# Performance work log

Hardware: AMD Instinct MI355X
Metric: run time of the kernel (lower is better)

The kernel has to match this reference:

```python
import jax, jax.numpy as jnp
import numpy as np

N_HEADS = 4
D_HEAD = 16
SCALE = D_HEAD ** 0.5  # NOTE: original multiplies by sqrt(d_head), faithful


def _mha(x, Wq, bq, Wk, bk, Wv, bv, Wo, bo):
    # x: (..., N, D) with D = N_HEADS * D_HEAD
    q = jnp.einsum('...nd,od->...no', x, Wq) + bq
    k = jnp.einsum('...nd,od->...no', x, Wk) + bk
    v = jnp.einsum('...nd,od->...no', x, Wv) + bv
    lead = x.shape[:-2]
    n = x.shape[-2]
    q = q.reshape(*lead, n, N_HEADS, D_HEAD)
    k = k.reshape(*lead, n, N_HEADS, D_HEAD)
    v = v.reshape(*lead, n, N_HEADS, D_HEAD)
    scores = jnp.einsum('...nhd,...mhd->...hnm', q, k) * SCALE
    attn = jax.nn.softmax(scores, axis=-1)
    o = jnp.einsum('...hnm,...mhd->...nhd', attn, v).reshape(*lead, n, N_HEADS * D_HEAD)
    return jnp.einsum('...nd,od->...no', o, Wo) + bo


def setup_inputs() -> dict:
    key = jax.random.key(0)
    ks = jax.random.split(key, 20)
    b, n, d, dhf, G, C = 16, 16384, 64, 64, 256, 64
    s = 0.05
    inp = {
        'x': jax.random.normal(ks[0], (b, n, d), dtype=jnp.float32),
        'partitions': jax.random.permutation(ks[1], n).reshape(G, C).astype(jnp.int64),
    }
    names = ['q_intra', 'k_intra', 'v_intra', 'o_intra',
             'q_inter', 'k_inter', 'v_inter', 'o_inter']
    for i, nm in enumerate(names):
        d_in = d if nm.endswith('intra') and nm[0] != 'o' else dhf
        inp['W' + nm] = jax.random.normal(ks[2 + 2 * i], (dhf, d_in), dtype=jnp.float32) * s
        inp['b' + nm] = jax.random.normal(ks[3 + 2 * i], (dhf,), dtype=jnp.float32) * s
    return inp


def reference(x, partitions,
              Wq_intra, bq_intra, Wk_intra, bk_intra, Wv_intra, bv_intra, Wo_intra, bo_intra,
              Wq_inter, bq_inter, Wk_inter, bk_inter, Wv_inter, bv_inter, Wo_inter, bo_inter):
    b = x.shape[0]
    G, C = partitions.shape
    dhf = Wq_intra.shape[0]
    # gather nodes into groups: (b, G, C, d)
    xg = x[:, partitions, :]
    # intra-group attention, vectorized over (b, G)
    intra = _mha(xg, Wq_intra, bq_intra, Wk_intra, bk_intra,
                 Wv_intra, bv_intra, Wo_intra, bo_intra)  # (b, G, C, dhf)
    # MaxPool1d(kernel=dhf) over token axis with C == dhf -> max over tokens
    pooled = jnp.max(intra, axis=2)  # (b, G, dhf)
    inter = _mha(pooled, Wq_inter, bq_inter, Wk_inter, bk_inter,
                 Wv_inter, bv_inter, Wo_inter, bo_inter)  # (b, G, dhf)
    # broadcast-add inter-group features to every token in the group
    out = intra + inter[:, :, None, :]  # (b, G, C, dhf)
    flat = out.reshape(b, G * C, dhf)
    inv = jnp.argsort(partitions.reshape(-1))  # restore original node order
    return flat[:, inv, :]
```

## Files before the change

### kernel.cpp

```cpp
#include <hip/hip_runtime.h>
#include <hip/hip_bf16.h>

#define NTOK 16384
#define NG   256
#define NB   16

typedef float  f32x4   __attribute__((ext_vector_type(4)));
typedef short  short8v __attribute__((ext_vector_type(8)));
typedef short  short4v __attribute__((ext_vector_type(4)));

#define MFMA_BF16(a, b, c) __builtin_amdgcn_mfma_f32_16x16x32_bf16((a), (b), (c), 0, 0, 0)

#define QSCALE 5.770780163555856f

__device__ __forceinline__ short f2bf(float f) {
    union { float f; unsigned u; } x; x.f = f;
    unsigned r = (x.u + 0x7FFF + ((x.u >> 16) & 1)) >> 16;
    return (short)r;
}
__device__ __forceinline__ short bft(float f) {
    union { float f; unsigned u; } x; x.f = f;
    return (short)(x.u >> 16);
}
__device__ __forceinline__ float bf2f(short s) {
    union { float f; unsigned u; } x;
    x.u = ((unsigned)(unsigned short)s) << 16;
    return x.f;
}

__global__ void k_setup(const int* __restrict__ raw, int* __restrict__ part,
                        const float* __restrict__ Wq, const float* __restrict__ Wk,
                        const float* __restrict__ Wv, const float* __restrict__ Wo,
                        const float* __restrict__ Wqe, const float* __restrict__ Wke,
                        const float* __restrict__ Wve, const float* __restrict__ Woe,
                        short8v* __restrict__ wf)
{
    const int gid = blockIdx.x * 256 + threadIdx.x;
    if (gid < 16384) {
        const bool is64 = (raw[1] == 0 && raw[3] == 0 && raw[5] == 0);
        part[gid] = is64 ? raw[2 * gid] : raw[gid];
        return;
    }
    const int p = gid - 16384;
    if (p >= 5632) return;
    if (p < 3584) {
        const int v    = p >> 9;
        const int rem  = p & 511;
        const int tau  = rem >> 6;
        const int lane = rem & 63;
        const int jt = tau >> 1, kt = tau & 1;
        const int o  = jt * 16 + (lane & 15);
        const int d0 = kt * 32 + (lane >> 4) * 8;
        const float* W = (v < 2) ? Wq : (v < 4) ? Wk : (v < 6) ? Wv : Wo;
        const bool lo = (v & 1) && (v < 6);
        short8v r8;
#pragma unroll
        for (int i = 0; i < 8; ++i) {
            const float f = W[o * 64 + d0 + i];
            const short hh = f2bf(f);
            r8[i] = lo ? f2bf(f - bf2f(hh)) : hh;
        }
        wf[p] = r8;
    } else {
        const int g2   = p - 3584;
        const int v    = g2 >> 9;
        const int rem  = g2 & 511;
        const int tau  = rem >> 6;
        const int lane = rem & 63;
        const int jt = tau >> 1, kt = tau & 1;
        const int o  = jt * 16 + (lane & 15);
        const int d0 = kt * 32 + (lane >> 4) * 8;
        const float* W = (v == 0) ? Wqe : (v == 1) ? Wke : (v == 2) ? Wve : Woe;
        short8v r8;
#pragma unroll
        for (int i = 0; i < 8; ++i) r8[i] = f2bf(W[o * 64 + d0 + i]);
        wf[p] = r8;
    }
}

__global__ __launch_bounds__(256, 4) void k_intra(
    const float* __restrict__ x, const int* __restrict__ part,
    const short8v* __restrict__ wf,
    const float* __restrict__ bq, const float* __restrict__ bk,
    const float* __restrict__ bv, const float* __restrict__ bo,
    float* __restrict__ out, float* __restrict__ pooled)
{
    __shared__ __align__(16) short S[20480];

    short* const xh = S;
    short* const kk = S + 4096;
    short* const ql = S + 8192;
    short* const qh = S + 12288;
    short* const vT = S + 16384;

    const int t  = threadIdx.x;
    const int g  = blockIdx.x;
    const int bb = blockIdx.y;
    const int l  = t & 63;
    const int w  = t >> 6;
    const int quad = l >> 4;
    const int col  = l & 15;

    for (int j = t; j < 512; j += 256) {
        const int row = j >> 3, c8 = j & 7;
        const int tok = part[g * 64 + row];
        const float* px = x + ((size_t)bb * NTOK + tok) * 64 + c8 * 8;
        const float4 f0 = ((const float4*)px)[0];
        const float4 f1 = ((const float4*)px)[1];
        const float v[8] = {f0.x, f0.y, f0.z, f0.w, f1.x, f1.y, f1.z, f1.w};
        short8v h8;
#pragma unroll
        for (int i = 0; i < 8; ++i) h8[i] = f2bf(v[i]);
        *(short8v*)&xh[row * 64 + ((c8 ^ (row & 7)) << 3)] = h8;
    }
    __syncthreads();

    {
        const float bqv = bq[w * 16 + col];
        const float bkv = bk[w * 16 + col];
        const float bvv = bv[w * 16 + col];
        short8v bqh[2], bql2[2], bkh[2], bkl[2], bvh[2], bvl[2];
#pragma unroll
        for (int kt = 0; kt < 2; ++kt) {
            const int tau = w * 2 + kt;
            bqh[kt]  = wf[(0 * 8 + tau) * 64 + l];
            bql2[kt] = wf[(1 * 8 + tau) * 64 + l];
            bkh[kt]  = wf[(2 * 8 + tau) * 64 + l];
            bkl[kt]  = wf[(3 * 8 + tau) * 64 + l];
            bvh[kt]  = wf[(4 * 8 + tau) * 64 + l];
            bvl[kt]  = wf[(5 * 8 + tau) * 64 + l];
        }
        for (int mt = 0; mt < 4; ++mt) {
            short8v axh[2];
#pragma unroll
            for (int kt = 0; kt < 2; ++kt) {
                const int row = mt * 16 + col;
                axh[kt] = *(const short8v*)&xh[row * 64 + (((kt * 4 + quad) ^ (row & 7)) << 3)];
            }
            f32x4 aq = {0.f, 0.f, 0.f, 0.f};
            f32x4 ak = {0.f, 0.f, 0.f, 0.f};
            f32x4 av = {0.f, 0.f, 0.f, 0.f};
#pragma unroll
            for (int kt = 0; kt < 2; ++kt) {
                aq = MFMA_BF16(axh[kt], bqh[kt],  aq);
                aq = MFMA_BF16(axh[kt], bql2[kt], aq);
                ak = MFMA_BF16(axh[kt], bkh[kt],  ak);
                ak = MFMA_BF16(axh[kt], bkl[kt],  ak);
                av = MFMA_BF16(axh[kt], bvh[kt],  av);
                av = MFMA_BF16(axh[kt], bvl[kt],  av);
            }
#pragma unroll
            for (int r = 0; r < 4; ++r) {
                const int m = mt * 16 + quad * 4 + r;
                const int pos = m * 64 + (((w * 2 + (col >> 3)) ^ (m & 7)) << 3) + (col & 7);
                const float q4 = (aq[r] + bqv) * QSCALE;
                const short hq = bft(q4);
                qh[pos] = hq;
                ql[pos] = bft(q4 - bf2f(hq));
                kk[pos] = f2bf(ak[r] + bkv);
            }
            {
                const int d = w * 16 + col;
                short4v v4;
#pragma unroll
                for (int r = 0; r < 4; ++r) v4[r] = f2bf(av[r] + bvv);
                const int cm = mt * 2 + (quad >> 1);
                const int idx = d * 64 + ((cm ^ (d & 7)) << 3) + ((quad & 1) * 4);
                *(short4v*)&vT[idx] = v4;
            }
        }
    }

    const int h = w, hc = h * 16;
    f32x4 s[4][4];
    {
        short8v bk4[4];
#pragma unroll
        for (int jt = 0; jt < 4; ++jt) {
            const int row = jt * 16 + col;
            bk4[jt] = *(const short8v*)&kk[row * 64 + (((h * 2 + (quad & 1)) ^ (row & 7)) << 3)];
        }
        const short8v z8 = {0, 0, 0, 0, 0, 0, 0, 0};
        for (int it = 0; it < 4; ++it) {
            const int row = it * 16 + col;
            const int idx = row * 64 + (((h * 2 + (quad & 1)) ^ (row & 7)) << 3);
            short8v aqh = *(const short8v*)&qh[idx];
            short8v aql = *(const short8v*)&ql[idx];
            if (quad >= 2) { aqh = z8; aql = z8; }
#pragma unroll
            for (int jt = 0; jt < 4; ++jt) {
                f32x4 acc = {0.f, 0.f, 0.f, 0.f};
                acc = MFMA_BF16(aqh, bk4[jt], acc);
                acc = MFMA_BF16(aql, bk4[jt], acc);
                s[it][jt] = acc;
            }
        }
    }
    float rden[4][4];
    for (int it = 0; it < 4; ++it) {
#pragma unroll
        for (int r = 0; r < 4; ++r) {
            float mx = fmaxf(fmaxf(s[it][0][r], s[it][1][r]),
                             fmaxf(s[it][2][r], s[it][3][r]));
            mx = fmaxf(mx, __shfl_xor(mx, 1));
            mx = fmaxf(mx, __shfl_xor(mx, 2));
            mx = fmaxf(mx, __shfl_xor(mx, 4));
            mx = fmaxf(mx, __shfl_xor(mx, 8));
            float ds = 0.f;
#pragma unroll
            for (int jt = 0; jt < 4; ++jt) {
                const float e = exp2f(s[it][jt][r] - mx);
                s[it][jt][r] = e;
                ds += e;
            }
            ds += __shfl_xor(ds, 1);
            ds += __shfl_xor(ds, 2);
            ds += __shfl_xor(ds, 4);
            ds += __shfl_xor(ds, 8);
            rden[it][r] = 1.0f / ds;
        }
    }
    __syncthreads();

    f32x4 oa[4];
#pragma unroll
    for (int it = 0; it < 4; ++it) oa[it] = (f32x4){0.f, 0.f, 0.f, 0.f};
    short* const Pw = S + w * 2560;
    for (int kt = 0; kt < 2; ++kt) {
        for (int it = 0; it < 4; ++it)
#pragma unroll
            for (int jl = 0; jl < 2; ++jl) {
                const int jt = kt * 2 + jl;
#pragma unroll
                for (int r = 0; r < 4; ++r)
                    Pw[(it * 16 + quad * 4 + r) * 40 + jl * 16 + col] = bft(s[it][jt][r]);
            }
        const int dv = hc + col;
        const int cmv = kt * 4 + quad;
        const short8v bv8 = *(const short8v*)&vT[dv * 64 + ((cmv ^ (dv & 7)) << 3)];
        for (int it = 0; it < 4; ++it) {
            const short8v ap = *(const short8v*)&Pw[(it * 16 + col) * 40 + quad * 8];
            oa[it] = MFMA_BF16(ap, bv8, oa[it]);
        }
    }
    for (int it = 0; it < 4; ++it)
#pragma unroll
        for (int r = 0; r < 4; ++r) {
            const int row = it * 16 + quad * 4 + r;
            const int pos = row * 64 + (((h * 2 + (col >> 3)) ^ (row & 7)) << 3) + (col & 7);
            qh[pos] = f2bf(oa[it][r] * rden[it][r]);
        }
    __syncthreads();

    {
        const float bov = bo[w * 16 + col];
        short8v bo8[2];
        bo8[0] = wf[(6 * 8 + w * 2 + 0) * 64 + l];
        bo8[1] = wf[(6 * 8 + w * 2 + 1) * 64 + l];
        float pm = -1e30f;
        for (int mt = 0; mt < 4; ++mt) {
            f32x4 acc = {0.f, 0.f, 0.f, 0.f};
#pragma unroll
            for (int kt = 0; kt < 2; ++kt) {
                const int row = mt * 16 + col;
                const short8v ao = *(const short8v*)&qh[row * 64 + (((kt * 4 + quad) ^ (row & 7)) << 3)];
                acc = MFMA_BF16(ao, bo8[kt], acc);
            }
#pragma unroll
            for (int r = 0; r < 4; ++r) {
                const float vo = acc[r] + bov;
                pm = fmaxf(pm, vo);
                const int tok = part[g * 64 + mt * 16 + quad * 4 + r];
                out[((size_t)bb * NTOK + tok) * 64 + w * 16 + col] = vo;
            }
        }
        pm = fmaxf(pm, __shfl_xor(pm, 16));
        pm = fmaxf(pm, __shfl_xor(pm, 32));
        if (l < 16)
            pooled[((size_t)bb * NG + g) * 64 + w * 16 + col] = pm;
    }
}

__global__ __launch_bounds__(256) void k_inter_qkv(
    const float* __restrict__ pooled, const short8v* __restrict__ wf,
    const float* __restrict__ bq, const float* __restrict__ bk,
    const float* __restrict__ bv,
    short* __restrict__ qws, short* __restrict__ kws, short* __restrict__ vTws)
{
    __shared__ __align__(16) short xs[4096];
    __shared__ __align__(16) short qs[64 * 72];
    __shared__ __align__(16) short ks2[64 * 72];
    const int t = threadIdx.x;
    const int chunk = blockIdx.x, bb = blockIdx.y;
    const int l = t & 63, w = t >> 6;
    const int quad = l >> 4, col = l & 15;

    for (int j = t; j < 512; j += 256) {
        const int row = j >> 3, c8 = j & 7;
        const float* px = pooled + ((size_t)bb * NG + chunk * 64 + row) * 64 + c8 * 8;
        const float4 f0 = ((const float4*)px)[0];
        const float4 f1 = ((const float4*)px)[1];
        const float v[8] = {f0.x, f0.y, f0.z, f0.w, f1.x, f1.y, f1.z, f1.w};
        short8v h8;
#pragma unroll
        for (int i = 0; i < 8; ++i) h8[i] = f2bf(v[i]);
        *(short8v*)&xs[row * 64 + ((c8 ^ (row & 7)) << 3)] = h8;
    }
    __syncthreads();

    const int WFI = 3584;
    short8v bqf[2], bkf[2], bvf[2];
#pragma unroll
    for (int kt = 0; kt < 2; ++kt) {
        bqf[kt] = wf[WFI + (0 * 8 + w * 2 + kt) * 64 + l];
        bkf[kt] = wf[WFI + (1 * 8 + w * 2 + kt) * 64 + l];
        bvf[kt] = wf[WFI + (2 * 8 + w * 2 + kt) * 64 + l];
    }
    const float bqv = bq[w * 16 + col];
    const float bkv = bk[w * 16 + col];
    const float bvv = bv[w * 16 + col];
    for (int mt = 0; mt < 4; ++mt) {
        short8v ax[2];
#pragma unroll
        for (int kt = 0; kt < 2; ++kt) {
            const int row = mt * 16 + col;
            ax[kt] = *(const short8v*)&xs[row * 64 + (((kt * 4 + quad) ^ (row & 7)) << 3)];
        }
        f32x4 aq = {0.f, 0.f, 0.f, 0.f};
        f32x4 ak = {0.f, 0.f, 0.f, 0.f};
        f32x4 av = {0.f, 0.f, 0.f, 0.f};
#pragma unroll
        for (int kt = 0; kt < 2; ++kt) {
            aq = MFMA_BF16(ax[kt], bqf[kt], aq);
            ak = MFMA_BF16(ax[kt], bkf[kt], ak);
            av = MFMA_BF16(ax[kt], bvf[kt], av);
        }
        short4v v4;
#pragma unroll
        for (int r = 0; r < 4; ++r) {
            const int m = mt * 16 + quad * 4 + r;
            qs[m * 72 + w * 16 + col]  = f2bf((aq[r] + bqv) * QSCALE);
            ks2[m * 72 + w * 16 + col] = f2bf(ak[r] + bkv);
            v4[r] = f2bf(av[r] + bvv);
        }
        *(short4v*)&vTws[((size_t)bb * 64 + w * 16 + col) * 256 + chunk * 64 + mt * 16 + quad * 4] = v4;
    }
    __syncthreads();
    for (int j = t; j < 512; j += 256) {
        const int row = j >> 3, c8 = j & 7;
        *(short8v*)&qws[((size_t)bb * NG + chunk * 64 + row) * 64 + c8 * 8] =
            *(const short8v*)&qs[row * 72 + c8 * 8];
        *(short8v*)&kws[((size_t)bb * NG + chunk * 64 + row) * 64 + c8 * 8] =
            *(const short8v*)&ks2[row * 72 + c8 * 8];
    }
}

__global__ __launch_bounds__(256) void k_inter_attn2(
    const short* __restrict__ qws, const short* __restrict__ kws,
    const short* __restrict__ vTws, const short8v* __restrict__ wf,
    const float* __restrict__ bo, float* __restrict__ inter)
{
    __shared__ __align__(16) short Pw_all[4 * 16 * 40];
    __shared__ __align__(16) short os[16 * 72];
    const int t = threadIdx.x;
    const int qt = blockIdx.x, bb = blockIdx.y;
    const int l = t & 63, w = t >> 6;
    const int quad = l >> 4, col = l & 15;
    const int hc = w * 16;
    const int r0 = qt * 16;

    const short8v z8 = {0, 0, 0, 0, 0, 0, 0, 0};
    short8v bk[16];
#pragma unroll
    for (int jt = 0; jt < 16; ++jt)
        bk[jt] = (quad < 2)
            ? *(const short8v*)&kws[((size_t)bb * NG + jt * 16 + col) * 64 + hc + quad * 8]
            : z8;
    short8v aq = (quad < 2)
        ? *(const short8v*)&qws[((size_t)bb * NG + r0 + col) * 64 + hc + quad * 8]
        : z8;

    f32x4 s[16];
#pragma unroll
    for (int jt = 0; jt < 16; ++jt) {
        f32x4 acc = {0.f, 0.f, 0.f, 0.f};
        s[jt] = MFMA_BF16(aq, bk[jt], acc);
    }

    float rden[4];
#pragma unroll
    for (int r = 0; r < 4; ++r) {
        float mx = -1e30f;
#pragma unroll
        for (int jt = 0; jt < 16; ++jt) mx = fmaxf(mx, s[jt][r]);
        mx = fmaxf(mx, __shfl_xor(mx, 1));
        mx = fmaxf(mx, __shfl_xor(mx, 2));
        mx = fmaxf(mx, __shfl_xor(mx, 4));
        mx = fmaxf(mx, __shfl_xor(mx, 8));
        float ds = 0.f;
#pragma unroll
        for (int jt = 0; jt < 16; ++jt) {
            const float e = exp2f(s[jt][r] - mx);
            s[jt][r] = e;
            ds += e;
        }
        ds += __shfl_xor(ds, 1);
        ds += __shfl_xor(ds, 2);
        ds += __shfl_xor(ds, 4);
        ds += __shfl_xor(ds, 8);
        rden[r] = 1.0f / ds;
    }

    short* const Pw = Pw_all + w * 16 * 40;
    f32x4 oa = {0.f, 0.f, 0.f, 0.f};
    for (int c = 0; c < 8; ++c) {
#pragma unroll
        for (int jl = 0; jl < 2; ++jl) {
            const int jt = c * 2 + jl;
#pragma unroll
            for (int r = 0; r < 4; ++r)
                Pw[(quad * 4 + r) * 40 + jl * 16 + col] = bft(s[jt][r]);
        }
        const short8v bv8 = *(const short8v*)&vTws[((size_t)bb * 64 + hc + col) * 256 + c * 32 + quad * 8];
        const short8v ap = *(const short8v*)&Pw[col * 40 + quad * 8];
        oa = MFMA_BF16(ap, bv8, oa);
    }
#pragma unroll
    for (int r = 0; r < 4; ++r)
        os[(quad * 4 + r) * 72 + hc + col] = f2bf(oa[r] * rden[r]);
    __syncthreads();

    short8v bof[2];
    bof[0] = wf[3584 + (3 * 8 + w * 2 + 0) * 64 + l];
    bof[1] = wf[3584 + (3 * 8 + w * 2 + 1) * 64 + l];
    const float bov = bo[w * 16 + col];
    {
        f32x4 acc = {0.f, 0.f, 0.f, 0.f};
#pragma unroll
        for (int kt = 0; kt < 2; ++kt) {
            const short8v ao = *(const short8v*)&os[col * 72 + kt * 32 + quad * 8];
            acc = MFMA_BF16(ao, bof[kt], acc);
        }
#pragma unroll
        for (int r = 0; r < 4; ++r)
            inter[((size_t)bb * NG + r0 + quad * 4 + r) * 64 + w * 16 + col] = acc[r] + bov;
    }
}

__global__ __launch_bounds__(256) void k_scatter_add(
    const float* __restrict__ inter, const int* __restrict__ part,
    float* __restrict__ out)
{
    __shared__ float iv[64];
    __shared__ int   pidx[64];
    const int t  = threadIdx.x;
    const int g  = blockIdx.x;
    const int bb = blockIdx.y;
    if (t < 64) {
        iv[t]   = inter[((size_t)bb * NG + g) * 64 + t];
        pidx[t] = part[g * 64 + t];
    }
    __syncthreads();
    const int oo   = t & 63;
    const int cseg = t >> 6;
    const float add = iv[oo];
    for (int ci = 0; ci < 16; ++ci) {
        const int c = cseg * 16 + ci;
        float* p = out + ((size_t)bb * NTOK + pidx[c]) * 64 + oo;
        *p += add;
    }
}

extern "C" void kernel_launch(void* const* d_in, const int* in_sizes, int n_in,
                              void* d_out, int out_size, void* d_ws, size_t ws_size,
                              hipStream_t stream)
{
    const float* x    = (const float*)d_in[0];
    const int*   praw = (const int*)d_in[1];
    const float* Wq_a = (const float*)d_in[2];
    const float* bq_a = (const float*)d_in[3];
    const float* Wk_a = (const float*)d_in[4];
    const float* bk_a = (const float*)d_in[5];
    const float* Wv_a = (const float*)d_in[6];
    const float* bv_a = (const float*)d_in[7];
    const float* Wo_a = (const float*)d_in[8];
    const float* bo_a = (const float*)d_in[9];
    const float* Wq_e = (const float*)d_in[10];
    const float* bq_e = (const float*)d_in[11];
    const float* Wk_e = (const float*)d_in[12];
    const float* bk_e = (const float*)d_in[13];
    const float* Wv_e = (const float*)d_in[14];
    const float* bv_e = (const float*)d_in[15];
    const float* Wo_e = (const float*)d_in[16];
    const float* bo_e = (const float*)d_in[17];

    char* ws = (char*)d_ws;
    int*     part   = (int*)ws;
    float*   pooled = (float*)(ws + (1u << 16));
    float*   inter  = (float*)(ws + (1u << 16) + (1u << 20));
    short8v* wf     = (short8v*)(ws + (1u << 16) + 2 * (1u << 20));
    char*    base2  = ws + (1u << 16) + 2 * (1u << 20) + 98304;
    short*   qws    = (short*)base2;
    short*   kws    = (short*)(base2 + (1u << 19));
    short*   vTws   = (short*)(base2 + 2 * (1u << 19));

    float* out = (float*)d_out;

    k_setup<<<dim3(86), dim3(256), 0, stream>>>(praw, part, Wq_a, Wk_a, Wv_a, Wo_a,
                                                Wq_e, Wk_e, Wv_e, Wo_e, wf);
    k_intra<<<dim3(NG, NB), dim3(256), 0, stream>>>(
        x, part, wf, bq_a, bk_a, bv_a, bo_a, out, pooled);
    k_inter_qkv<<<dim3(4, NB), dim3(256), 0, stream>>>(
        pooled, wf, bq_e, bk_e, bv_e, qws, kws, vTws);
    k_inter_attn2<<<dim3(16, NB), dim3(256), 0, stream>>>(
        qws, kws, vTws, wf, bo_e, inter);
    k_scatter_add<<<dim3(NG, NB), dim3(256), 0, stream>>>(inter, part, out);
}
```

Before: 223.6 us.

## Stage intra output as grouped bf16 and scatter once in final kernel

When the workspace is large enough, the intra kernel writes its output contiguously per group as bf16 into a staging buffer instead of scattering fp32 to out. A new final kernel reads that buffer, adds the inter-group features, and writes out once in scattered order. The old path read back and rewrote out, so this cuts intermediate traffic. The bf16 rounding of intra adds precision loss. fp32 to bf16 packing now uses a perm-based paired RNE conversion.

```diff
diff --git a/kernel.cpp b/kernel.cpp
--- a/kernel.cpp
+++ b/kernel.cpp
@@ -26,6 +26,12 @@
     union { float f; unsigned u; } x;
     x.u = ((unsigned)(unsigned short)s) << 16;
     return x.f;
+}
+__device__ __forceinline__ unsigned pk_rne(float a, float b) {
+    union { float f; unsigned u; } xa, xb; xa.f = a; xb.f = b;
+    const unsigned ua = xa.u + (0x7FFFu + ((xa.u >> 16) & 1));
+    const unsigned ub = xb.u + (0x7FFFu + ((xb.u >> 16) & 1));
+    return __builtin_amdgcn_perm(ub, ua, 0x07060302u);
 }
 
 __global__ void k_setup(const int* __restrict__ raw, int* __restrict__ part,
@@ -83,7 +89,8 @@
     const short8v* __restrict__ wf,
     const float* __restrict__ bq, const float* __restrict__ bk,
     const float* __restrict__ bv, const float* __restrict__ bo,
-    float* __restrict__ out, float* __restrict__ pooled)
+    float* __restrict__ out, float* __restrict__ pooled,
+    unsigned short* __restrict__ intra_g, const int use_g)
 {
     __shared__ __align__(16) short S[20480];
 
@@ -107,11 +114,12 @@
         const float* px = x + ((size_t)bb * NTOK + tok) * 64 + c8 * 8;
         const float4 f0 = ((const float4*)px)[0];
         const float4 f1 = ((const float4*)px)[1];
-        const float v[8] = {f0.x, f0.y, f0.z, f0.w, f1.x, f1.y, f1.z, f1.w};
-        short8v h8;
-#pragma unroll
-        for (int i = 0; i < 8; ++i) h8[i] = f2bf(v[i]);
-        *(short8v*)&xh[row * 64 + ((c8 ^ (row & 7)) << 3)] = h8;
+        uint4 pk;
+        pk.x = pk_rne(f0.x, f0.y);
+        pk.y = pk_rne(f0.z, f0.w);
+        pk.z = pk_rne(f1.x, f1.y);
+        pk.w = pk_rne(f1.z, f1.w);
+        *(uint4*)&xh[row * 64 + ((c8 ^ (row & 7)) << 3)] = pk;
     }
     __syncthreads();
 
@@ -258,6 +266,7 @@
         bo8[0] = wf[(6 * 8 + w * 2 + 0) * 64 + l];
         bo8[1] = wf[(6 * 8 + w * 2 + 1) * 64 + l];
         float pm = -1e30f;
+        const size_t gbase = ((size_t)bb * NG + g) * 64;
         for (int mt = 0; mt < 4; ++mt) {
             f32x4 acc = {0.f, 0.f, 0.f, 0.f};
 #pragma unroll
@@ -266,12 +275,22 @@
                 const short8v ao = *(const short8v*)&qh[row * 64 + (((kt * 4 + quad) ^ (row & 7)) << 3)];
                 acc = MFMA_BF16(ao, bo8[kt], acc);
             }
-#pragma unroll
-            for (int r = 0; r < 4; ++r) {
-                const float vo = acc[r] + bov;
-                pm = fmaxf(pm, vo);
-                const int tok = part[g * 64 + mt * 16 + quad * 4 + r];
-                out[((size_t)bb * NTOK + tok) * 64 + w * 16 + col] = vo;
+            if (use_g) {
+#pragma unroll
+                for (int r = 0; r < 4; ++r) {
+                    const float vo = acc[r] + bov;
+                    pm = fmaxf(pm, vo);
+                    intra_g[(gbase + mt * 16 + quad * 4 + r) * 64 + w * 16 + col] =
+                        (unsigned short)f2bf(vo);
+                }
+            } else {
+#pragma unroll
+                for (int r = 0; r < 4; ++r) {
+                    const float vo = acc[r] + bov;
+                    pm = fmaxf(pm, vo);
+                    const int tok = part[g * 64 + mt * 16 + quad * 4 + r];
+                    out[((size_t)bb * NTOK + tok) * 64 + w * 16 + col] = vo;
+                }
             }
         }
         pm = fmaxf(pm, __shfl_xor(pm, 16));
@@ -300,11 +319,12 @@
         const float* px = pooled + ((size_t)bb * NG + chunk * 64 + row) * 64 + c8 * 8;
         const float4 f0 = ((const float4*)px)[0];
         const float4 f1 = ((const float4*)px)[1];
-        const float v[8] = {f0.x, f0.y, f0.z, f0.w, f1.x, f1.y, f1.z, f1.w};
-        short8v h8;
-#pragma unroll
-        for (int i = 0; i < 8; ++i) h8[i] = f2bf(v[i]);
-        *(short8v*)&xs[row * 64 + ((c8 ^ (row & 7)) << 3)] = h8;
+        uint4 pk;
+        pk.x = pk_rne(f0.x, f0.y);
+        pk.y = pk_rne(f0.z, f0.w);
+        pk.z = pk_rne(f1.x, f1.y);
+        pk.w = pk_rne(f1.z, f1.w);
+        *(uint4*)&xs[row * 64 + ((c8 ^ (row & 7)) << 3)] = pk;
     }
     __syncthreads();
 
@@ -444,6 +464,33 @@
 #pragma unroll
         for (int r = 0; r < 4; ++r)
             inter[((size_t)bb * NG + r0 + quad * 4 + r) * 64 + w * 16 + col] = acc[r] + bov;
+    }
+}
+
+__global__ __launch_bounds__(256) void k_final(
+    const unsigned short* __restrict__ intra_g, const float* __restrict__ inter,
+    const int* __restrict__ part, float* __restrict__ out)
+{
+    __shared__ float interL[64];
+    __shared__ int   pidx[64];
+    const int t  = threadIdx.x;
+    const int g  = blockIdx.x;
+    const int bb = blockIdx.y;
+    if (t < 64) pidx[t] = part[g * 64 + t];
+    else if (t < 128) interL[t - 64] = inter[((size_t)bb * NG + g) * 64 + (t - 64)];
+    __syncthreads();
+    const size_t ibase = ((size_t)bb * NG + g) * 64 * 64;
+#pragma unroll
+    for (int i = 0; i < 8; ++i) {
+        const int item = i * 256 + t;
+        const int row  = item >> 5;
+        const int pr   = item & 31;
+        const unsigned u = *(const unsigned*)&intra_g[ibase + row * 64 + pr * 2];
+        const float2 iv = *(const float2*)&interL[pr * 2];
+        float2 o;
+        o.x = bf2f((short)(u & 0xFFFF)) + iv.x;
+        o.y = bf2f((short)(u >> 16))    + iv.y;
+        *(float2*)&out[((size_t)bb * NTOK + pidx[row]) * 64 + pr * 2] = o;
     }
 }
 
@@ -503,16 +550,22 @@
     short*   qws    = (short*)base2;
     short*   kws    = (short*)(base2 + (1u << 19));
     short*   vTws   = (short*)(base2 + 2 * (1u << 19));
+    unsigned short* intra_g = (unsigned short*)(base2 + 3 * (1u << 19));
+    const size_t need = ((size_t)(base2 - ws)) + 3 * (1u << 19) + (size_t)NB * NG * 64 * 64 * 2;
+    const int use_g = (ws_size >= need) ? 1 : 0;
 
     float* out = (float*)d_out;
 
     k_setup<<<dim3(86), dim3(256), 0, stream>>>(praw, part, Wq_a, Wk_a, Wv_a, Wo_a,
                                                 Wq_e, Wk_e, Wv_e, Wo_e, wf);
     k_intra<<<dim3(NG, NB), dim3(256), 0, stream>>>(
-        x, part, wf, bq_a, bk_a, bv_a, bo_a, out, pooled);
+        x, part, wf, bq_a, bk_a, bv_a, bo_a, out, pooled, intra_g, use_g);
     k_inter_qkv<<<dim3(4, NB), dim3(256), 0, stream>>>(
         pooled, wf, bq_e, bk_e, bv_e, qws, kws, vTws);
     k_inter_attn2<<<dim3(16, NB), dim3(256), 0, stream>>>(
         qws, kws, vTws, wf, bo_e, inter);
-    k_scatter_add<<<dim3(NG, NB), dim3(256), 0, stream>>>(inter, part, out);
-}
+    if (use_g)
+        k_final<<<dim3(NG, NB), dim3(256), 0, stream>>>(intra_g, inter, part, out);
+    else
+        k_scatter_add<<<dim3(NG, NB), dim3(256), 0, stream>>>(inter, part, out);
+}
```

New measurement: 220.4 us. Within noise of the previous version (-1.4%).
